# Optimization experiments

Hardware: AMD Instinct MI355X
Metric: run time of the kernel (lower is better)

The kernel has to match this reference:

```python
import jax, jax.numpy as jnp
import numpy as np

T, N, C, D = 64, 32, 128, 64   # timesteps, batch, vector_dim, jeffress_dim
FD = (32, 32)                  # feature_dims of sqrt_model
TAU_F = 2.0                    # SynapseFilter tau (and jeffress integrator tau)
LIF_TAU = 20.0                 # jeffress LIFNode tau


def setup_inputs() -> dict:
    key = jax.random.key(0)
    ks = jax.random.split(key, 6)
    # binary spike trains, 2 input channels
    x = (jax.random.uniform(ks[0], (T, N, 2, C)) < 0.2).astype(jnp.float32)
    def w(k, o, i):
        return (jax.random.normal(k, (o, i)) / np.sqrt(i)).astype(jnp.float32)
    return {
        'x': x,
        'w1': w(ks[1], 10, 1),  'b1': jnp.zeros((10,), jnp.float32),
        'w2': w(ks[2], 1, 10),  'b2': jnp.zeros((1,), jnp.float32),
        'sw0': w(ks[3], FD[0], 1),      'sb0': jnp.zeros((FD[0],), jnp.float32),
        'sw1': w(ks[4], FD[1], FD[0]),  'sb1': jnp.zeros((FD[1],), jnp.float32),
        'sw2': w(ks[5], 1, FD[1]),      'sb2': jnp.zeros((1,), jnp.float32),
    }


def _spike(v):
    # IF/LIF fire: heaviside(v - v_threshold), v_threshold = 1.0
    return (v >= 1.0).astype(v.dtype)


def _forward(x, w1, b1, w2, b2, sw0, sb0, sw1, sb1, sw2, sb2, spike):
    x = jnp.swapaxes(x, 2, 3)            # (T,N,C,2)
    x0, x1 = x[..., 0], x[..., 1]        # (T,N,C) two delay-line inputs
    # JeffressLinear: coincidence detection, unit j sees x0 delayed by j and
    # x1 delayed by D-1-j:  u[t, ..., j] = x0[t-j] + x1[t-(D-1-j)]
    pad = jnp.zeros((D - 1, N, C), x.dtype)
    xp0 = jnp.concatenate([pad, x0], axis=0)   # (T+D-1,N,C)
    xp1 = jnp.concatenate([pad, x1], axis=0)
    tt = jnp.arange(T)[:, None]
    jj = jnp.arange(D)[None, :]
    u = xp0[tt + (D - 1) - jj] + xp1[tt + jj]  # (T,D,N,C)
    u = jnp.moveaxis(u, 1, -1)                 # (T,N,C,D)

    # fixed jeffress_integrator kernel: 1/(1 - exp(-|d|/tau))
    dist = jnp.arange(D) - D // 2
    kint = 1.0 / (1.0 - jnp.exp(-jnp.abs(dist) / TAU_F))
    # center (d=0) is inf in the original; clamp to nearest-neighbor weight
    kint = jnp.where(dist == 0, 1.0 / (1.0 - jnp.exp(-1.0 / TAU_F)), kint)

    z = lambda s: jnp.zeros(s, jnp.float32)
    st0 = (z((N, C, D)), z((N, C, 1)),              # jeffress LIF v, integrator IF v
           z((N, C, 1)), z((N, C, 10)), z((N, C, 10)), z((N, C, 1)),  # square: f1,v1,f2,v2
           z((N, C)), z((N, 1)),                    # sum filter, sum IF v
           z((N, 1)), z((N, FD[0])),                # sqrt: g0, q0
           z((N, FD[0])), z((N, FD[1])),            # g1, q1
           z((N, FD[1])), z((N, 1)))                # g2, q2 (NonSpikingIF)

    def step(st, ut):
        vj, vi, f1, v1, f2, v2, fs, vs, g0, q0, g1, q1, g2, q2 = st
        # jeffress LIF (tau=20, decay_input, hard reset to 0)
        vj = vj + (ut - vj) / LIF_TAU
        s = spike(vj); vj = (1.0 - s) * vj
        # fixed integrator linear D -> 1, then IF neuron
        zc = jnp.einsum('ncd,d->nc', s, kint)[..., None]   # (N,C,1)
        vi = vi + zc; s = spike(vi); vi = (1.0 - s) * vi
        # square_model: filter -> Linear(1,10) -> IF -> filter -> Linear(10,1) -> IF
        f1 = f1 - f1 / TAU_F + s
        v1 = v1 + f1 @ w1.T + b1; s = spike(v1); v1 = (1.0 - s) * v1
        f2 = f2 - f2 / TAU_F + s
        v2 = v2 + f2 @ w2.T + b2; s = spike(v2); v2 = (1.0 - s) * v2
        # flatten, sum filter, sum over C, sum IF neuron
        fs = fs - fs / TAU_F + s[..., 0]
        vs = vs + fs.sum(axis=1, keepdims=True)
        s = spike(vs); vs = (1.0 - s) * vs
        # sqrt_model operates on detached spikes
        h = jax.lax.stop_gradient(s)                       # (N,1)
        g0 = g0 - g0 / TAU_F + h
        q0 = q0 + h @ sw0.T + sb0; s = spike(q0); q0 = (1.0 - s) * q0
        g1 = g1 - g1 / TAU_F + s
        q1 = q1 + g1 @ sw1.T + sb1; s = spike(q1); q1 = (1.0 - s) * q1
        g2 = g2 - g2 / TAU_F + s
        q2 = q2 + g2 @ sw2.T + sb2                         # NonSpikingIF: output = v
        return (vj, vi, f1, v1, f2, v2, fs, vs, g0, q0, g1, q1, g2, q2), q2

    _, out = jax.lax.scan(step, st0, u)
    return out   # (T,N,1)


def reference(x, w1, b1, w2, b2, sw0, sb0, sw1, sb1, sw2, sb2):
    return _forward(x, w1, b1, w2, b2, sw0, sb0, sw1, sb1, sw2, sb2, _spike)
```

## Files before the change

### kernel.cpp

```cpp
#include <hip/hip_runtime.h>
#include <math.h>

typedef unsigned long long ull;

#define TT 64
#define NN 32
#define CC 128
#define DD 64

#define DPPADD(x, ctrl, rm)                                                   \
    x += __builtin_bit_cast(float, __builtin_amdgcn_update_dpp(               \
             0, __builtin_bit_cast(int, x), ctrl, rm, 0xf, false))

__device__ __forceinline__ float wave_reduce63(float x) {
    DPPADD(x, 0x111, 0xf);
    DPPADD(x, 0x112, 0xf);
    DPPADD(x, 0x114, 0xf);
    DPPADD(x, 0x118, 0xf);
    DPPADD(x, 0x142, 0xa);
    DPPADD(x, 0x143, 0xc);
    return x;
}

__device__ __forceinline__ float rdlane(float x, int l) {
    return __builtin_bit_cast(float,
        __builtin_amdgcn_readlane(__builtin_bit_cast(int, x), l));
}
__device__ __forceinline__ float bit2f(unsigned m, int j) {
    return __builtin_bit_cast(float, (0u - ((m >> j) & 1u)) & 0x3f800000u);
}

__global__ __launch_bounds__(1024) void kAB(
    const float* __restrict__ x,
    const float* __restrict__ w1,  const float* __restrict__ b1,
    const float* __restrict__ w2,  const float* __restrict__ b2,
    float* __restrict__ fsbuf)
{
#pragma clang fp contract(off)
    __shared__ ull   maskLds[16];
    __shared__ float fsl[16][TT + 1];

    const int tid  = threadIdx.x;
    const int lane = tid & 63;
    const int w    = tid >> 6;
    const int wid  = (blockIdx.x << 4) + w;
    const int n = wid >> 7;
    const int c = wid & 127;

    {
        const float x0 = x[((lane * NN + n) * 2 + 0) * CC + c];
        const float x1 = x[((lane * NN + n) * 2 + 1) * CC + c];
        const ull m0 = __ballot(x0 > 0.5f) << lane;
        const ull m1 = __ballot(x1 > 0.5f) << (63 - lane);
        const unsigned m0lo = (unsigned)m0, m0hi = (unsigned)(m0 >> 32);
        const unsigned m1lo = (unsigned)m1, m1hi = (unsigned)(m1 >> 32);

        int ad = lane - (DD / 2);
        if (ad < 0) ad = -ad;
        if (ad == 0) ad = 1;
        const float kint = 1.0f / (1.0f - expf(-(float)ad * 0.5f));

        const float R = 0.05f;
        float vj = 0.f;
        unsigned rlo = 0u, rhi = 0u;

#pragma unroll
        for (int t = 0; t < 13; ++t) {
            const unsigned b0 = (m0lo >> t) & 1u;
            const unsigned b1b = (m1lo >> t) & 1u;
            const float u = (float)(b0 + b1b);
            const float num = u - vj;
            const float q0  = num * R;
            vj = vj + fmaf(fmaf(-20.0f, q0, num), R, q0);
        }

#pragma unroll
        for (int t = 13; t < TT; ++t) {
            const unsigned b0 = (t < 32) ? ((m0lo >> t) & 1u) : ((m0hi >> (t - 32)) & 1u);
            const unsigned b1b = (t < 32) ? ((m1lo >> t) & 1u) : ((m1hi >> (t - 32)) & 1u);
            const float u = (float)(b0 + b1b);

            const float num = u - vj;
            const float q0  = num * R;
            const float q   = fmaf(fmaf(-20.0f, q0, num), R, q0);
            vj = vj + q;

            const bool sp = vj >= 1.0f;
            const ull m = __ballot(sp);
            vj = sp ? 0.0f : vj;
            if (t == lane) { rlo = (unsigned)m; rhi = (unsigned)(m >> 32); }
        }

        float zc = 0.f;
#pragma unroll
        for (int d = 0; d < 64; ++d) {
            const float kd = rdlane(kint, d);
            const unsigned bit = (d < 32) ? ((rlo >> d) & 1u) : ((rhi >> (d - 32)) & 1u);
            zc = fmaf((float)bit, kd, zc);
        }

        float vi = 0.f, sreg = 0.f;
#pragma unroll
        for (int t = 13; t < TT; ++t) {
            vi += rdlane(zc, t);
            const bool sp = vi >= 1.0f;
            const float siF = sp ? 1.0f : 0.0f;
            vi = sp ? 0.0f : vi;
            if (t == lane) sreg = siF;
        }
        const ull mm = __ballot(sreg > 0.5f);
        if (lane == 0) maskLds[w] = mm;
    }
    __syncthreads();

    if (tid < 256) {
        const int g   = tid & 15;
        const int cib = tid >> 4;

        const ull mm = maskLds[cib];
        const unsigned mlo = (unsigned)mm, mhi = (unsigned)(mm >> 32);

        const int k = (g < 10) ? g : 0;
        const float W1k = w1[k], B1k = b1[k];
        const float W2k = (g < 10) ? w2[k] : 0.0f;
        const float B2  = b2[0];

        float f1 = 0.f, v1 = 0.f, f2 = 0.f, v2 = 0.f, fs = 0.f;

#pragma unroll
        for (int t = 0; t < TT; ++t) {
            const float si = (float)((t < 32) ? ((mlo >> t) & 1u)
                                              : ((mhi >> (t - 32)) & 1u));
            f1 = f1 * 0.5f + si;

            v1 = v1 + (f1 * W1k + B1k);
            const bool s1b = v1 >= 1.0f;
            const float s1 = s1b ? 1.0f : 0.0f;
            v1 = s1b ? 0.0f : v1;

            f2 = f2 * 0.5f + s1;
            float acc = f2 * W2k;
            acc += __shfl_xor(acc, 1);
            acc += __shfl_xor(acc, 2);
            acc += __shfl_xor(acc, 4);
            acc += __shfl_xor(acc, 8);

            v2 = v2 + (acc + B2);
            const bool s2b = v2 >= 1.0f;
            const float s2 = s2b ? 1.0f : 0.0f;
            v2 = s2b ? 0.0f : v2;

            fs = fs * 0.5f + s2;
            fsl[cib][t] = fs;
        }
    }
    __syncthreads();

    if (tid < 256) {
        float* dst = fsbuf + (blockIdx.x << 10);
#pragma unroll
        for (int i = tid; i < 16 * TT; i += 256)
            dst[i] = fsl[i >> 6][i & 63];
    }
}

__global__ __launch_bounds__(64) void kB2_v17(
    const float* __restrict__ fsbuf,
    const float* __restrict__ sw0, const float* __restrict__ sb0,
    const float* __restrict__ sw1, const float* __restrict__ sb1,
    const float* __restrict__ sw2, const float* __restrict__ sb2,
    float* __restrict__ out)
{
#pragma clang fp contract(off)
    const int n = blockIdx.x;
    const int tid = threadIdx.x;
    const int k = tid & 31;
    const int h = tid >> 5;

    const float* base = fsbuf + n * (CC * TT);
    float a0 = 0.f, a1 = 0.f, a2 = 0.f, a3 = 0.f;
#pragma unroll
    for (int c = 0; c < CC; c += 4) {
        a0 += base[(c + 0) * TT + tid];
        a1 += base[(c + 1) * TT + tid];
        a2 += base[(c + 2) * TT + tid];
        a3 += base[(c + 3) * TT + tid];
    }
    const float sums = (a0 + a1) + (a2 + a3);

    const float SW0 = sw0[k], SB0 = sb0[k], SB1 = sb1[k];
    float SW1[16];
#pragma unroll
    for (int j = 0; j < 16; ++j) SW1[j] = sw1[k * 32 + h * 16 + j];
    const float SW2j = (tid < 32) ? sw2[k] : 0.0f;
    const float SB2 = sb2[0];

    const bool zb0 = (__ballot(SB0 == 0.0f) == ~0ull);

    float vs = 0.f, q0 = 0.f, q1 = 0.f, g2 = 0.f, q2 = 0.f;
    float g1loc[16];
#pragma unroll
    for (int j = 0; j < 16; ++j) g1loc[j] = 0.f;
    float ptot = 0.f;
    float pvs  = 0.f;
    int   L    = 0;

#pragma unroll 4
    for (int t = 0; t < TT; ++t) {
        const float p = rdlane(sums, t);
        vs += p;
        const bool spv = vs >= 1.0f;
        vs = spv ? 0.0f : vs;
        const float s = spv ? 1.0f : 0.0f;

        unsigned m;
        if (spv || !zb0) {
            q0 = q0 + fmaf(s, SW0, SB0);
            const bool sp0 = q0 >= 1.0f;
            q0 = sp0 ? 0.0f : q0;
            m = (unsigned)__ballot(sp0);
        } else {
            m = 0u;
        }

        if (m != 0) {
            if (L) {
                const float sc = __builtin_bit_cast(float,
                                     (unsigned)(127 - L) << 23);
#pragma unroll
                for (int j = 0; j < 16; ++j) g1loc[j] *= sc;
                L = 0;
            }
#pragma unroll
            for (int j = 0; j < 16; ++j)
                g1loc[j] = fmaf(g1loc[j], 0.5f, bit2f(m, h * 16 + j));

            float b0 = 0.f, b1v = 0.f, b2a = 0.f, b3 = 0.f;
#pragma unroll
            for (int j = 0; j < 16; j += 4) {
                b0  += SW1[j + 0] * g1loc[j + 0];
                b1v += SW1[j + 1] * g1loc[j + 1];
                b2a += SW1[j + 2] * g1loc[j + 2];
                b3  += SW1[j + 3] * g1loc[j + 3];
            }
            float part = (b0 + b1v) + (b2a + b3);
            part += __shfl_xor(part, 32);
            ptot = part;
        } else {
            ++L;
            ptot = 0.5f * ptot;
        }

        q1 = q1 + (ptot + SB1);
        const bool sp1 = q1 >= 1.0f;
        const float s1 = sp1 ? 1.0f : 0.0f;
        q1 = sp1 ? 0.0f : q1;

        const unsigned m2 = (unsigned)__ballot(sp1);

        g2 = fmaf(g2, 0.5f, s1);

        if (m2 != 0) {
            float pv = g2 * SW2j;
            pv = wave_reduce63(pv);
            pvs = rdlane(pv, 63);
        } else {
            pvs = 0.5f * pvs;
        }

        q2 = q2 + (pvs + SB2);
        if (tid == 0) out[t * NN + n] = q2;
    }
}

extern "C" void kernel_launch(void* const* d_in, const int* in_sizes, int n_in,
                              void* d_out, int out_size, void* d_ws, size_t ws_size,
                              hipStream_t stream)
{
    const float* x   = (const float*)d_in[0];
    const float* w1  = (const float*)d_in[1];
    const float* b1  = (const float*)d_in[2];
    const float* w2  = (const float*)d_in[3];
    const float* b2  = (const float*)d_in[4];
    const float* sw0 = (const float*)d_in[5];
    const float* sb0 = (const float*)d_in[6];
    const float* sw1 = (const float*)d_in[7];
    const float* sb1 = (const float*)d_in[8];
    const float* sw2 = (const float*)d_in[9];
    const float* sb2 = (const float*)d_in[10];
    float* out = (float*)d_out;

    float* fsbuf = (float*)d_ws;

    hipLaunchKernelGGL(kAB, dim3((NN * CC) / 16), dim3(1024), 0, stream,
                       x, w1, b1, w2, b2, fsbuf);
    hipLaunchKernelGGL(kB2_v17, dim3(NN), dim3(64), 0, stream,
                       fsbuf, sw0, sb0, sw1, sb1, sw2, sb2, out);
}
```

Before: 34.58 us.

## Fuse both kernels into one launch with per-block flag synchronization

Merges the spike-encoding kernel and the sqrt_model scan kernel into a single launch. The extra 32 consumer blocks spin on per-producer release/acquire flags in workspace before reducing fsbuf, and reset the flags afterwards. This removes the second kernel launch and the inter-kernel gap. In exchange, the consumers rely on the producer blocks being scheduled, and the flags must start zeroed in the workspace. Consumer blocks also request 1024 threads while only 64 do work.

Measured after the change: 53.94 us. 56.0% more time.

```diff
diff --git a/kernel.cpp b/kernel.cpp
--- a/kernel.cpp
+++ b/kernel.cpp
@@ -7,6 +7,7 @@
 #define NN 32
 #define CC 128
 #define DD 64
+#define MAGIC 0x13572468u
 
 #define DPPADD(x, ctrl, rm)                                                   \
     x += __builtin_bit_cast(float, __builtin_amdgcn_update_dpp(               \
@@ -30,152 +31,167 @@
     return __builtin_bit_cast(float, (0u - ((m >> j) & 1u)) & 0x3f800000u);
 }
 
-__global__ __launch_bounds__(1024) void kAB(
+__global__ __launch_bounds__(1024) void kFused(
     const float* __restrict__ x,
     const float* __restrict__ w1,  const float* __restrict__ b1,
     const float* __restrict__ w2,  const float* __restrict__ b2,
-    float* __restrict__ fsbuf)
+    const float* __restrict__ sw0, const float* __restrict__ sb0,
+    const float* __restrict__ sw1, const float* __restrict__ sb1,
+    const float* __restrict__ sw2, const float* __restrict__ sb2,
+    float* __restrict__ fsbuf,
+    unsigned* __restrict__ flags,
+    float* __restrict__ out)
 {
 #pragma clang fp contract(off)
     __shared__ ull   maskLds[16];
     __shared__ float fsl[16][TT + 1];
 
     const int tid  = threadIdx.x;
-    const int lane = tid & 63;
-    const int w    = tid >> 6;
-    const int wid  = (blockIdx.x << 4) + w;
-    const int n = wid >> 7;
-    const int c = wid & 127;
-
-    {
-        const float x0 = x[((lane * NN + n) * 2 + 0) * CC + c];
-        const float x1 = x[((lane * NN + n) * 2 + 1) * CC + c];
-        const ull m0 = __ballot(x0 > 0.5f) << lane;
-        const ull m1 = __ballot(x1 > 0.5f) << (63 - lane);
-        const unsigned m0lo = (unsigned)m0, m0hi = (unsigned)(m0 >> 32);
-        const unsigned m1lo = (unsigned)m1, m1hi = (unsigned)(m1 >> 32);
-
-        int ad = lane - (DD / 2);
-        if (ad < 0) ad = -ad;
-        if (ad == 0) ad = 1;
-        const float kint = 1.0f / (1.0f - expf(-(float)ad * 0.5f));
-
-        const float R = 0.05f;
-        float vj = 0.f;
-        unsigned rlo = 0u, rhi = 0u;
-
-#pragma unroll
-        for (int t = 0; t < 13; ++t) {
-            const unsigned b0 = (m0lo >> t) & 1u;
-            const unsigned b1b = (m1lo >> t) & 1u;
-            const float u = (float)(b0 + b1b);
-            const float num = u - vj;
-            const float q0  = num * R;
-            vj = vj + fmaf(fmaf(-20.0f, q0, num), R, q0);
-        }
-
-#pragma unroll
-        for (int t = 13; t < TT; ++t) {
-            const unsigned b0 = (t < 32) ? ((m0lo >> t) & 1u) : ((m0hi >> (t - 32)) & 1u);
-            const unsigned b1b = (t < 32) ? ((m1lo >> t) & 1u) : ((m1hi >> (t - 32)) & 1u);
-            const float u = (float)(b0 + b1b);
-
-            const float num = u - vj;
-            const float q0  = num * R;
-            const float q   = fmaf(fmaf(-20.0f, q0, num), R, q0);
-            vj = vj + q;
-
-            const bool sp = vj >= 1.0f;
-            const ull m = __ballot(sp);
-            vj = sp ? 0.0f : vj;
-            if (t == lane) { rlo = (unsigned)m; rhi = (unsigned)(m >> 32); }
-        }
-
-        float zc = 0.f;
-#pragma unroll
-        for (int d = 0; d < 64; ++d) {
-            const float kd = rdlane(kint, d);
-            const unsigned bit = (d < 32) ? ((rlo >> d) & 1u) : ((rhi >> (d - 32)) & 1u);
-            zc = fmaf((float)bit, kd, zc);
-        }
-
-        float vi = 0.f, sreg = 0.f;
-#pragma unroll
-        for (int t = 13; t < TT; ++t) {
-            vi += rdlane(zc, t);
-            const bool sp = vi >= 1.0f;
-            const float siF = sp ? 1.0f : 0.0f;
-            vi = sp ? 0.0f : vi;
-            if (t == lane) sreg = siF;
-        }
-        const ull mm = __ballot(sreg > 0.5f);
-        if (lane == 0) maskLds[w] = mm;
+
+    if (blockIdx.x < 256) {
+        const int lane = tid & 63;
+        const int w    = tid >> 6;
+        const int wid  = (blockIdx.x << 4) + w;
+        const int n = wid >> 7;
+        const int c = wid & 127;
+
+        {
+            const float x0 = x[((lane * NN + n) * 2 + 0) * CC + c];
+            const float x1 = x[((lane * NN + n) * 2 + 1) * CC + c];
+            const ull m0 = __ballot(x0 > 0.5f) << lane;
+            const ull m1 = __ballot(x1 > 0.5f) << (63 - lane);
+            const unsigned m0lo = (unsigned)m0, m0hi = (unsigned)(m0 >> 32);
+            const unsigned m1lo = (unsigned)m1, m1hi = (unsigned)(m1 >> 32);
+
+            int ad = lane - (DD / 2);
+            if (ad < 0) ad = -ad;
+            if (ad == 0) ad = 1;
+            const float kint = 1.0f / (1.0f - expf(-(float)ad * 0.5f));
+
+            const float R = 0.05f;
+            float vj = 0.f;
+            unsigned rlo = 0u, rhi = 0u;
+
+#pragma unroll
+            for (int t = 0; t < 13; ++t) {
+                const unsigned b0 = (m0lo >> t) & 1u;
+                const unsigned b1b = (m1lo >> t) & 1u;
+                const float u = (float)(b0 + b1b);
+                const float num = u - vj;
+                const float q0  = num * R;
+                vj = vj + fmaf(fmaf(-20.0f, q0, num), R, q0);
+            }
+
+#pragma unroll
+            for (int t = 13; t < TT; ++t) {
+                const unsigned b0 = (t < 32) ? ((m0lo >> t) & 1u) : ((m0hi >> (t - 32)) & 1u);
+                const unsigned b1b = (t < 32) ? ((m1lo >> t) & 1u) : ((m1hi >> (t - 32)) & 1u);
+                const float u = (float)(b0 + b1b);
+
+                const float num = u - vj;
+                const float q0  = num * R;
+                const float q   = fmaf(fmaf(-20.0f, q0, num), R, q0);
+                vj = vj + q;
+
+                const bool sp = vj >= 1.0f;
+                const ull m = __ballot(sp);
+                vj = sp ? 0.0f : vj;
+                if (t == lane) { rlo = (unsigned)m; rhi = (unsigned)(m >> 32); }
+            }
+
+            float zc = 0.f;
+#pragma unroll
+            for (int d = 0; d < 64; ++d) {
+                const float kd = rdlane(kint, d);
+                const unsigned bit = (d < 32) ? ((rlo >> d) & 1u) : ((rhi >> (d - 32)) & 1u);
+                zc = fmaf((float)bit, kd, zc);
+            }
+
+            float vi = 0.f, sreg = 0.f;
+#pragma unroll
+            for (int t = 13; t < TT; ++t) {
+                vi += rdlane(zc, t);
+                const bool sp = vi >= 1.0f;
+                const float siF = sp ? 1.0f : 0.0f;
+                vi = sp ? 0.0f : vi;
+                if (t == lane) sreg = siF;
+            }
+            const ull mm = __ballot(sreg > 0.5f);
+            if (lane == 0) maskLds[w] = mm;
+        }
+        __syncthreads();
+
+        if (tid < 256) {
+            const int g   = tid & 15;
+            const int cib = tid >> 4;
+
+            const ull mm = maskLds[cib];
+            const unsigned mlo = (unsigned)mm, mhi = (unsigned)(mm >> 32);
+
+            const int k = (g < 10) ? g : 0;
+            const float W1k = w1[k], B1k = b1[k];
+            const float W2k = (g < 10) ? w2[k] : 0.0f;
+            const float B2  = b2[0];
+
+            float f1 = 0.f, v1 = 0.f, f2 = 0.f, v2 = 0.f, fs = 0.f;
+
+#pragma unroll
+            for (int t = 0; t < TT; ++t) {
+                const float si = (float)((t < 32) ? ((mlo >> t) & 1u)
+                                                  : ((mhi >> (t - 32)) & 1u));
+                f1 = f1 * 0.5f + si;
+
+                v1 = v1 + (f1 * W1k + B1k);
+                const bool s1b = v1 >= 1.0f;
+                const float s1 = s1b ? 1.0f : 0.0f;
+                v1 = s1b ? 0.0f : v1;
+
+                f2 = f2 * 0.5f + s1;
+                float acc = f2 * W2k;
+                acc += __shfl_xor(acc, 1);
+                acc += __shfl_xor(acc, 2);
+                acc += __shfl_xor(acc, 4);
+                acc += __shfl_xor(acc, 8);
+
+                v2 = v2 + (acc + B2);
+                const bool s2b = v2 >= 1.0f;
+                const float s2 = s2b ? 1.0f : 0.0f;
+                v2 = s2b ? 0.0f : v2;
+
+                fs = fs * 0.5f + s2;
+                fsl[cib][t] = fs;
+            }
+        }
+        __syncthreads();
+
+        if (tid < 256) {
+            float* dst = fsbuf + (blockIdx.x << 10);
+#pragma unroll
+            for (int i = tid; i < 16 * TT; i += 256)
+                dst[i] = fsl[i >> 6][i & 63];
+        }
+        __syncthreads();
+
+        if (tid == 0) {
+            __threadfence();
+            __hip_atomic_store(&flags[blockIdx.x], MAGIC,
+                               __ATOMIC_RELEASE, __HIP_MEMORY_SCOPE_AGENT);
+        }
+        return;
     }
-    __syncthreads();
-
-    if (tid < 256) {
-        const int g   = tid & 15;
-        const int cib = tid >> 4;
-
-        const ull mm = maskLds[cib];
-        const unsigned mlo = (unsigned)mm, mhi = (unsigned)(mm >> 32);
-
-        const int k = (g < 10) ? g : 0;
-        const float W1k = w1[k], B1k = b1[k];
-        const float W2k = (g < 10) ? w2[k] : 0.0f;
-        const float B2  = b2[0];
-
-        float f1 = 0.f, v1 = 0.f, f2 = 0.f, v2 = 0.f, fs = 0.f;
-
-#pragma unroll
-        for (int t = 0; t < TT; ++t) {
-            const float si = (float)((t < 32) ? ((mlo >> t) & 1u)
-                                              : ((mhi >> (t - 32)) & 1u));
-            f1 = f1 * 0.5f + si;
-
-            v1 = v1 + (f1 * W1k + B1k);
-            const bool s1b = v1 >= 1.0f;
-            const float s1 = s1b ? 1.0f : 0.0f;
-            v1 = s1b ? 0.0f : v1;
-
-            f2 = f2 * 0.5f + s1;
-            float acc = f2 * W2k;
-            acc += __shfl_xor(acc, 1);
-            acc += __shfl_xor(acc, 2);
-            acc += __shfl_xor(acc, 4);
-            acc += __shfl_xor(acc, 8);
-
-            v2 = v2 + (acc + B2);
-            const bool s2b = v2 >= 1.0f;
-            const float s2 = s2b ? 1.0f : 0.0f;
-            v2 = s2b ? 0.0f : v2;
-
-            fs = fs * 0.5f + s2;
-            fsl[cib][t] = fs;
-        }
-    }
-    __syncthreads();
-
-    if (tid < 256) {
-        float* dst = fsbuf + (blockIdx.x << 10);
-#pragma unroll
-        for (int i = tid; i < 16 * TT; i += 256)
-            dst[i] = fsl[i >> 6][i & 63];
-    }
-}
-
-__global__ __launch_bounds__(64) void kB2_v17(
-    const float* __restrict__ fsbuf,
-    const float* __restrict__ sw0, const float* __restrict__ sb0,
-    const float* __restrict__ sw1, const float* __restrict__ sb1,
-    const float* __restrict__ sw2, const float* __restrict__ sb2,
-    float* __restrict__ out)
-{
-#pragma clang fp contract(off)
-    const int n = blockIdx.x;
-    const int tid = threadIdx.x;
+
+    if (tid >= 64) return;
+
+    const int n = blockIdx.x - 256;
     const int k = tid & 31;
     const int h = tid >> 5;
+
+    if (tid < 8) {
+        while (__hip_atomic_load(&flags[n * 8 + tid],
+                                 __ATOMIC_ACQUIRE, __HIP_MEMORY_SCOPE_AGENT)
+               != MAGIC)
+            __builtin_amdgcn_s_sleep(8);
+    }
 
     const float* base = fsbuf + n * (CC * TT);
     float a0 = 0.f, a1 = 0.f, a2 = 0.f, a3 = 0.f;
@@ -271,6 +287,10 @@
         q2 = q2 + (pvs + SB2);
         if (tid == 0) out[t * NN + n] = q2;
     }
+
+    if (tid < 8)
+        __hip_atomic_store(&flags[n * 8 + tid], 0u,
+                           __ATOMIC_RELAXED, __HIP_MEMORY_SCOPE_AGENT);
 }
 
 extern "C" void kernel_launch(void* const* d_in, const int* in_sizes, int n_in,
@@ -290,10 +310,10 @@
     const float* sb2 = (const float*)d_in[10];
     float* out = (float*)d_out;
 
-    float* fsbuf = (float*)d_ws;
-
-    hipLaunchKernelGGL(kAB, dim3((NN * CC) / 16), dim3(1024), 0, stream,
-                       x, w1, b1, w2, b2, fsbuf);
-    hipLaunchKernelGGL(kB2_v17, dim3(NN), dim3(64), 0, stream,
-                       fsbuf, sw0, sb0, sw1, sb1, sw2, sb2, out);
-}
+    float*    fsbuf = (float*)d_ws;
+    unsigned* flags = (unsigned*)((char*)d_ws + (1 << 20));
+
+    hipLaunchKernelGGL(kFused, dim3(256 + NN), dim3(1024), 0, stream,
+                       x, w1, b1, w2, b2, sw0, sb0, sw1, sb1, sw2, sb2,
+                       fsbuf, flags, out);
+}
```
